# Performance work log

Measured on AMD Instinct MI355X. Metric: run time of the kernel, lower is better.

The kernel has to match this reference:

```python
import jax, jax.numpy as jnp
import numpy as np

N = 8192        # num nodes (bs in the original docstring)
D_IN = 512      # input feature dim
HEADS = 8
DPH = 512 // HEADS  # size_per_head = hidden_size // num_heads
EDGE_P = 0.01   # adjacency density


def setup_inputs() -> dict:
    key = jax.random.key(0)
    k1, k2, k3 = jax.random.split(key, 3)
    H = jax.random.normal(k1, (N, D_IN), dtype=jnp.float32)
    # dense 0/1 adjacency, as passed to the layer before tf.sparse.from_dense
    adj = (jax.random.uniform(k2, (N, N)) < EDGE_P).astype(jnp.float32)
    # Glorot-uniform per-head projection kernels, stacked: (HEADS, D_IN, DPH)
    limit = float(np.sqrt(6.0 / (D_IN + DPH)))
    W = jax.random.uniform(k3, (HEADS, D_IN, DPH), jnp.float32, -limit, limit)
    b = jnp.zeros((HEADS, DPH), jnp.float32)
    return {"H": H, "adj": adj, "W": W, "b": b}


def reference(H, adj, W, b):
    # Per-head dense projection: H_ = H @ W_h  -> (HEADS, N, DPH)
    H_ = jnp.einsum('nd,hde->hne', H, W)
    # NOTE: the original layer computes a sparse sigmoid/softmax attention
    # (f1 + f2^T over adj) but never uses it: head_output uses raw adj.
    # Aggregation: adj @ H_ per head, plus bias; activation = tf.identity.
    out = jnp.einsum('nm,hme->hne', adj, H_) + b[:, None, :]  # (HEADS, N, DPH)
    # Concat heads along feature axis (head 0 first) -> (N, HEADS*DPH)
    return jnp.transpose(out, (1, 0, 2)).reshape(H.shape[0], HEADS * DPH)
```

## Files before the change

### kernel.cpp

```cpp
#include <hip/hip_runtime.h>
#include <hip/hip_bf16.h>

typedef __attribute__((ext_vector_type(8))) short short8;
typedef __attribute__((ext_vector_type(4))) float floatx4;

#define GN 8192
#define GD 512
#define MAXDEG 256
#define GEMM_BLOCKS 512

static __device__ __forceinline__ ushort bf16bits(float x) {
  __hip_bfloat16 h = __float2bfloat16(x);
  return *(ushort*)&h;
}
static __device__ __forceinline__ float bf16f(uint u16) {
  return __uint_as_float(u16 << 16);
}

__global__ void detect_kernel(const uint* __restrict__ H, const uint* __restrict__ W,
                              const uint* __restrict__ adj, const uint* __restrict__ b,
                              int* __restrict__ flags, float* __restrict__ bias) {
  __shared__ int cH, cW, cA, cB;
  const int t = threadIdx.x;
  if (t == 0) { cH = 0; cW = 0; cA = 0; cB = 0; }
  __syncthreads();
  { const uint e = (H[t] >> 7) & 0xFFu; if (e >= 100u && e <= 140u) atomicAdd(&cH, 1); }
  { const uint e = (W[t] >> 7) & 0xFFu; if (e >= 100u && e <= 140u) atomicAdd(&cW, 1); }
  for (int i = t; i < 4096; i += 256)
    if ((adj[i] & 0xFFFFu) == 0x3F80u) atomicAdd(&cA, 1);
  if (b[t] != 0u) atomicAdd(&cB, 1);
  __syncthreads();
  const int hb = cH > 128, wb = cW > 128, ab = cA > 0;
  if (t == 0) { flags[0] = hb; flags[1] = wb; flags[2] = ab; }
  if (cB == 0) {
    bias[t] = 0.0f; bias[t + 256] = 0.0f;
  } else if (wb) {
    const ushort* bs = (const ushort*)b;
    bias[t] = bf16f(bs[t]); bias[t + 256] = bf16f(bs[t + 256]);
  } else {
    const float* bf = (const float*)b;
    bias[t] = bf[t]; bias[t + 256] = bf[t + 256];
  }
}

#define BM 128
#define BN 64
#define BK 64
#define LDK 72

#define SMEM_BYTES (BM * LDK * 2 + BN * LDK * 2)

__global__ __launch_bounds__(256) void fused_kernel(
    const void* __restrict__ Hv, const void* __restrict__ Wv,
    const void* __restrict__ adjv, ushort* __restrict__ HP,
    int* __restrict__ rowcnt, uint2* __restrict__ edges,
    const int* __restrict__ flags) {
  __shared__ __align__(16) unsigned char smem[SMEM_BYTES];

  const int tid = threadIdx.x;

  if (blockIdx.x < GEMM_BLOCKS) {
    ushort* sA = (ushort*)smem;
    ushort* sB = (ushort*)(smem + BM * LDK * 2);
    const int hb = flags[0];
    const int wb = flags[1];
    const int bn = blockIdx.x & 7;
    const int bm = blockIdx.x >> 3;
    const int m0 = bm * BM;
    const int lane = tid & 63;
    const int w = tid >> 6;
    const int wr = w >> 1, wc = w & 1;
    const int l15 = lane & 15, q = lane >> 4;

    floatx4 acc[4][2];
#pragma unroll
    for (int i = 0; i < 4; i++)
#pragma unroll
      for (int j = 0; j < 2; j++) acc[i][j] = (floatx4)0.0f;

    for (int k0 = 0; k0 < GD; k0 += BK) {
      __syncthreads();
      if (hb) {
        const ushort* H16 = (const ushort*)Hv;
        const int r = tid >> 3;
        const int kc = (tid & 7) * 8;
#pragma unroll
        for (int p = 0; p < 4; p++) {
          const int row = r + p * 32;
          const uint4 v = *(const uint4*)(H16 + (size_t)(m0 + row) * GD + k0 + kc);
          *(uint4*)(sA + row * LDK + kc) = v;
        }
      } else {
        const float* H32 = (const float*)Hv;
        const int r0 = tid >> 4;
        const int kc = (tid & 15) * 4;
#pragma unroll
        for (int p = 0; p < 8; p++) {
          const int row = r0 + p * 16;
          const float4 v = *(const float4*)(H32 + (size_t)(m0 + row) * GD + k0 + kc);
          ushort4 o;
          o.x = bf16bits(v.x); o.y = bf16bits(v.y);
          o.z = bf16bits(v.z); o.w = bf16bits(v.w);
          *(ushort4*)(sA + row * LDK + kc) = o;
        }
      }
      if (wb) {
        const ushort* Wh = (const ushort*)Wv + (size_t)bn * (512 * 64);
        const int kk = tid >> 3;
        const int e0 = (tid & 7) * 8;
#pragma unroll
        for (int p = 0; p < 2; p++) {
          const int k = kk + p * 32;
          const uint4 v = *(const uint4*)(Wh + (size_t)(k0 + k) * 64 + e0);
          const ushort* pv = (const ushort*)&v;
#pragma unroll
          for (int j = 0; j < 8; j++) sB[(e0 + j) * LDK + k] = pv[j];
        }
      } else {
        const float* Wh = (const float*)Wv + (size_t)bn * (512 * 64);
        const int kk = tid >> 4;
        const int e0 = (tid & 15) * 4;
#pragma unroll
        for (int p = 0; p < 4; p++) {
          const int k = kk + p * 16;
          const float4 v = *(const float4*)(Wh + (size_t)(k0 + k) * 64 + e0);
          sB[(e0 + 0) * LDK + k] = bf16bits(v.x);
          sB[(e0 + 1) * LDK + k] = bf16bits(v.y);
          sB[(e0 + 2) * LDK + k] = bf16bits(v.z);
          sB[(e0 + 3) * LDK + k] = bf16bits(v.w);
        }
      }
      __syncthreads();
#pragma unroll
      for (int kq = 0; kq < 2; kq++) {
        short8 af[4], bfv[2];
#pragma unroll
        for (int mt = 0; mt < 4; mt++)
          af[mt] = *(const short8*)(sA + (wr * 64 + mt * 16 + l15) * LDK + kq * 32 + q * 8);
#pragma unroll
        for (int ct = 0; ct < 2; ct++)
          bfv[ct] = *(const short8*)(sB + (wc * 32 + ct * 16 + l15) * LDK + kq * 32 + q * 8);
#pragma unroll
        for (int mt = 0; mt < 4; mt++)
#pragma unroll
          for (int ct = 0; ct < 2; ct++)
            acc[mt][ct] = __builtin_amdgcn_mfma_f32_16x16x32_bf16(
                af[mt], bfv[ct], acc[mt][ct], 0, 0, 0);
      }
    }
#pragma unroll
    for (int mt = 0; mt < 4; mt++)
#pragma unroll
      for (int ct = 0; ct < 2; ct++)
#pragma unroll
        for (int r = 0; r < 4; r++) {
          const int row = m0 + wr * 64 + mt * 16 + q * 4 + r;
          const int col = bn * 64 + wc * 32 + ct * 16 + l15;
          HP[(size_t)row * GD + col] = bf16bits(acc[mt][ct][r]);
        }
  } else {
    int* s_idx = (int*)smem;
    float* s_val = (float*)(smem + 1024);
    int* s_cnt = (int*)(smem + 2048);
    const int ab = flags[2];
    const int n = blockIdx.x - GEMM_BLOCKS;
    const int t = tid;
    if (t == 0) *s_cnt = 0;
    __syncthreads();
    if (ab) {
      const ushort* arow = (const ushort*)adjv + (size_t)n * GN;
#pragma unroll
      for (int c = 0; c < 8; c++) {
        const int c0 = c * 1024;
        const uint2 v = *(const uint2*)(arow + c0 + t * 4);
        const uint e[4] = {v.x & 0xFFFFu, v.x >> 16, v.y & 0xFFFFu, v.y >> 16};
#pragma unroll
        for (int j = 0; j < 4; j++)
          if (e[j] != 0u) {
            const int pos = atomicAdd(s_cnt, 1);
            if (pos < MAXDEG) { s_idx[pos] = c0 + t * 4 + j; s_val[pos] = bf16f(e[j]); }
          }
      }
    } else {
      const float* arow = (const float*)adjv + (size_t)n * GN;
#pragma unroll
      for (int c = 0; c < 8; c++) {
        const int c0 = c * 1024;
        const float4 v = *(const float4*)(arow + c0 + t * 4);
        const float pv[4] = {v.x, v.y, v.z, v.w};
#pragma unroll
        for (int j = 0; j < 4; j++)
          if (pv[j] != 0.0f) {
            const int pos = atomicAdd(s_cnt, 1);
            if (pos < MAXDEG) { s_idx[pos] = c0 + t * 4 + j; s_val[pos] = pv[j]; }
          }
      }
    }
    __syncthreads();
    const int cnt = min(*s_cnt, MAXDEG);
    if (t == 0) rowcnt[n] = cnt;
    if (t < cnt) {
      uint2 e; e.x = (uint)s_idx[t]; e.y = __float_as_uint(s_val[t]);
      edges[(size_t)n * MAXDEG + t] = e;
    }
  }
}

__global__ __launch_bounds__(128) void gather_kernel(
    const ushort* __restrict__ HP, const int* __restrict__ rowcnt,
    const uint2* __restrict__ edges, const float* __restrict__ bias,
    float* __restrict__ out) {
  __shared__ int s_idx[MAXDEG];
  __shared__ float s_val[MAXDEG];

  const int b = blockIdx.x;
  const int half = b & 1;
  const int n = b >> 1;
  const int t = threadIdx.x;
  const int cnt = rowcnt[n];

  for (int i = t; i < cnt; i += 128) {
    const uint2 e = edges[(size_t)n * MAXDEG + i];
    s_idx[i] = (int)e.x;
    s_val[i] = __uint_as_float(e.y);
  }
  __syncthreads();

  const uint* HPu = (const uint*)HP;
  const int co = (half << 7) + t;
  float acc0 = 0.0f, acc1 = 0.0f;
  int i = 0;
  for (; i + 4 <= cnt; i += 4) {
    const int m0_ = s_idx[i + 0], m1_ = s_idx[i + 1];
    const int m2_ = s_idx[i + 2], m3_ = s_idx[i + 3];
    const float v0 = s_val[i + 0], v1 = s_val[i + 1];
    const float v2 = s_val[i + 2], v3 = s_val[i + 3];
    const uint u0 = HPu[(size_t)m0_ * 256 + co];
    const uint u1 = HPu[(size_t)m1_ * 256 + co];
    const uint u2 = HPu[(size_t)m2_ * 256 + co];
    const uint u3 = HPu[(size_t)m3_ * 256 + co];
    acc0 += v0 * bf16f(u0 & 0xFFFFu) + v1 * bf16f(u1 & 0xFFFFu);
    acc0 += v2 * bf16f(u2 & 0xFFFFu) + v3 * bf16f(u3 & 0xFFFFu);
    acc1 += v0 * __uint_as_float(u0 & 0xFFFF0000u) + v1 * __uint_as_float(u1 & 0xFFFF0000u);
    acc1 += v2 * __uint_as_float(u2 & 0xFFFF0000u) + v3 * __uint_as_float(u3 & 0xFFFF0000u);
  }
  for (; i < cnt; i++) {
    const int m_ = s_idx[i];
    const float vv = s_val[i];
    const uint u = HPu[(size_t)m_ * 256 + co];
    acc0 += vv * bf16f(u & 0xFFFFu);
    acc1 += vv * __uint_as_float(u & 0xFFFF0000u);
  }

  const float2 bb = ((const float2*)bias)[co];
  float2 o;
  o.x = acc0 + bb.x;
  o.y = acc1 + bb.y;
  ((float2*)out)[(size_t)n * 256 + co] = o;
}

extern "C" void kernel_launch(void* const* d_in, const int* in_sizes, int n_in,
                              void* d_out, int out_size, void* d_ws, size_t ws_size,
                              hipStream_t stream) {
  const void *H = d_in[0], *adj = d_in[1], *W = d_in[2], *b = d_in[3];
  for (int i = 0; i < n_in; i++) {
    const int s = in_sizes[i];
    if (s == GN * GN) adj = d_in[i];
    else if (s == GN * GD) H = d_in[i];
    else if (s == 8 * 512 * 64) W = d_in[i];
    else if (s == 512) b = d_in[i];
  }
  float* out = (float*)d_out;

  char* ws = (char*)d_ws;
  ushort* HP   = (ushort*)ws;
  float*  bias = (float*)(ws + (size_t)GN * GD * 2);
  int*    flags= (int*)(ws + (size_t)GN * GD * 2 + 2048);
  int*  rowcnt = (int*)(ws + (size_t)GN * GD * 2 + 4096);
  uint2* edges = (uint2*)(ws + (size_t)GN * GD * 2 + 4096 + GN * 4);

  detect_kernel<<<1, 256, 0, stream>>>((const uint*)H, (const uint*)W,
                                       (const uint*)adj, (const uint*)b,
                                       flags, bias);
  fused_kernel<<<GEMM_BLOCKS + GN, 256, 0, stream>>>(H, W, adj, HP,
                                                     rowcnt, edges, flags);
  gather_kernel<<<GN * 2, 128, 0, stream>>>(HP, rowcnt, edges, bias, out);
}
```

Before: 432.1 us.

## Split projected features into half-width planes and gather one row per wavefront

The GEMM now writes the bf16 projection into two separate half-width arrays (columns 0-255 and 256-511), so each half-row is a contiguous 512-byte segment. The gather kernel is restructured so that each 64-lane wavefront handles one node's half-row. Each lane loads a uint2 (4 bf16 values) per neighbour and stores a float4, and edges are staged in a per-wave shared buffer with no block barrier. This aims to cut the gather's block count and barrier overhead and to widen memory transactions per neighbour row. The trade-off is fewer in-flight loads per output element and slightly higher register pressure.

```diff
diff --git a/kernel.cpp b/kernel.cpp
--- a/kernel.cpp
+++ b/kernel.cpp
@@ -52,9 +52,9 @@
 
 __global__ __launch_bounds__(256) void fused_kernel(
     const void* __restrict__ Hv, const void* __restrict__ Wv,
-    const void* __restrict__ adjv, ushort* __restrict__ HP,
-    int* __restrict__ rowcnt, uint2* __restrict__ edges,
-    const int* __restrict__ flags) {
+    const void* __restrict__ adjv, ushort* __restrict__ HPlo,
+    ushort* __restrict__ HPhi, int* __restrict__ rowcnt,
+    uint2* __restrict__ edges, const int* __restrict__ flags) {
   __shared__ __align__(16) unsigned char smem[SMEM_BYTES];
 
   const int tid = threadIdx.x;
@@ -148,6 +148,8 @@
                 af[mt], bfv[ct], acc[mt][ct], 0, 0, 0);
       }
     }
+    ushort* HPdst = (bn < 4) ? HPlo : HPhi;
+    const int cbase = (bn & 3) * 64;
 #pragma unroll
     for (int mt = 0; mt < 4; mt++)
 #pragma unroll
@@ -155,8 +157,8 @@
 #pragma unroll
         for (int r = 0; r < 4; r++) {
           const int row = m0 + wr * 64 + mt * 16 + q * 4 + r;
-          const int col = bn * 64 + wc * 32 + ct * 16 + l15;
-          HP[(size_t)row * GD + col] = bf16bits(acc[mt][ct][r]);
+          const int col = cbase + wc * 32 + ct * 16 + l15;
+          HPdst[(size_t)row * 256 + col] = bf16bits(acc[mt][ct][r]);
         }
   } else {
     int* s_idx = (int*)smem;
@@ -206,57 +208,58 @@
   }
 }
 
-__global__ __launch_bounds__(128) void gather_kernel(
-    const ushort* __restrict__ HP, const int* __restrict__ rowcnt,
-    const uint2* __restrict__ edges, const float* __restrict__ bias,
-    float* __restrict__ out) {
-  __shared__ int s_idx[MAXDEG];
-  __shared__ float s_val[MAXDEG];
+__global__ __launch_bounds__(256) void gather_kernel(
+    const ushort* __restrict__ HPlo, const ushort* __restrict__ HPhi,
+    const int* __restrict__ rowcnt, const uint2* __restrict__ edges,
+    const float* __restrict__ bias, float* __restrict__ out) {
+  __shared__ uint2 s_e[4][MAXDEG];
 
   const int b = blockIdx.x;
   const int half = b & 1;
-  const int n = b >> 1;
-  const int t = threadIdx.x;
+  const int w = threadIdx.x >> 6;
+  const int lane = threadIdx.x & 63;
+  const int n = (b >> 1) * 4 + w;
+
   const int cnt = rowcnt[n];
-
-  for (int i = t; i < cnt; i += 128) {
-    const uint2 e = edges[(size_t)n * MAXDEG + i];
-    s_idx[i] = (int)e.x;
-    s_val[i] = __uint_as_float(e.y);
-  }
-  __syncthreads();
-
-  const uint* HPu = (const uint*)HP;
-  const int co = (half << 7) + t;
-  float acc0 = 0.0f, acc1 = 0.0f;
+  for (int i = lane; i < cnt; i += 64)
+    s_e[w][i] = edges[(size_t)n * MAXDEG + i];
+
+  const uint2* HPsrc = (const uint2*)(half ? HPhi : HPlo);
+  float a0 = 0.f, a1 = 0.f, a2 = 0.f, a3 = 0.f;
+
   int i = 0;
   for (; i + 4 <= cnt; i += 4) {
-    const int m0_ = s_idx[i + 0], m1_ = s_idx[i + 1];
-    const int m2_ = s_idx[i + 2], m3_ = s_idx[i + 3];
-    const float v0 = s_val[i + 0], v1 = s_val[i + 1];
-    const float v2 = s_val[i + 2], v3 = s_val[i + 3];
-    const uint u0 = HPu[(size_t)m0_ * 256 + co];
-    const uint u1 = HPu[(size_t)m1_ * 256 + co];
-    const uint u2 = HPu[(size_t)m2_ * 256 + co];
-    const uint u3 = HPu[(size_t)m3_ * 256 + co];
-    acc0 += v0 * bf16f(u0 & 0xFFFFu) + v1 * bf16f(u1 & 0xFFFFu);
-    acc0 += v2 * bf16f(u2 & 0xFFFFu) + v3 * bf16f(u3 & 0xFFFFu);
-    acc1 += v0 * __uint_as_float(u0 & 0xFFFF0000u) + v1 * __uint_as_float(u1 & 0xFFFF0000u);
-    acc1 += v2 * __uint_as_float(u2 & 0xFFFF0000u) + v3 * __uint_as_float(u3 & 0xFFFF0000u);
+    const uint2 e0 = s_e[w][i + 0], e1 = s_e[w][i + 1];
+    const uint2 e2 = s_e[w][i + 2], e3 = s_e[w][i + 3];
+    const uint2 u0 = HPsrc[(size_t)e0.x * 64 + lane];
+    const uint2 u1 = HPsrc[(size_t)e1.x * 64 + lane];
+    const uint2 u2 = HPsrc[(size_t)e2.x * 64 + lane];
+    const uint2 u3 = HPsrc[(size_t)e3.x * 64 + lane];
+    const float v0 = __uint_as_float(e0.y), v1 = __uint_as_float(e1.y);
+    const float v2 = __uint_as_float(e2.y), v3 = __uint_as_float(e3.y);
+    a0 += v0 * bf16f(u0.x & 0xFFFFu) + v1 * bf16f(u1.x & 0xFFFFu)
+        + v2 * bf16f(u2.x & 0xFFFFu) + v3 * bf16f(u3.x & 0xFFFFu);
+    a1 += v0 * __uint_as_float(u0.x & 0xFFFF0000u) + v1 * __uint_as_float(u1.x & 0xFFFF0000u)
+        + v2 * __uint_as_float(u2.x & 0xFFFF0000u) + v3 * __uint_as_float(u3.x & 0xFFFF0000u);
+    a2 += v0 * bf16f(u0.y & 0xFFFFu) + v1 * bf16f(u1.y & 0xFFFFu)
+        + v2 * bf16f(u2.y & 0xFFFFu) + v3 * bf16f(u3.y & 0xFFFFu);
+    a3 += v0 * __uint_as_float(u0.y & 0xFFFF0000u) + v1 * __uint_as_float(u1.y & 0xFFFF0000u)
+        + v2 * __uint_as_float(u2.y & 0xFFFF0000u) + v3 * __uint_as_float(u3.y & 0xFFFF0000u);
   }
   for (; i < cnt; i++) {
-    const int m_ = s_idx[i];
-    const float vv = s_val[i];
-    const uint u = HPu[(size_t)m_ * 256 + co];
-    acc0 += vv * bf16f(u & 0xFFFFu);
-    acc1 += vv * __uint_as_float(u & 0xFFFF0000u);
-  }
-
-  const float2 bb = ((const float2*)bias)[co];
-  float2 o;
-  o.x = acc0 + bb.x;
-  o.y = acc1 + bb.y;
-  ((float2*)out)[(size_t)n * 256 + co] = o;
+    const uint2 e = s_e[w][i];
+    const float v = __uint_as_float(e.y);
+    const uint2 u = HPsrc[(size_t)e.x * 64 + lane];
+    a0 += v * bf16f(u.x & 0xFFFFu);
+    a1 += v * __uint_as_float(u.x & 0xFFFF0000u);
+    a2 += v * bf16f(u.y & 0xFFFFu);
+    a3 += v * __uint_as_float(u.y & 0xFFFF0000u);
+  }
+
+  const float4 bb = ((const float4*)bias)[half * 64 + lane];
+  float4 o;
+  o.x = a0 + bb.x; o.y = a1 + bb.y; o.z = a2 + bb.z; o.w = a3 + bb.w;
+  ((float4*)out)[(size_t)n * 128 + half * 64 + lane] = o;
 }
 
 extern "C" void kernel_launch(void* const* d_in, const int* in_sizes, int n_in,
@@ -273,7 +276,8 @@
   float* out = (float*)d_out;
 
   char* ws = (char*)d_ws;
-  ushort* HP   = (ushort*)ws;
+  ushort* HPlo = (ushort*)ws;
+  ushort* HPhi = (ushort*)(ws + (size_t)GN * 256 * 2);
   float*  bias = (float*)(ws + (size_t)GN * GD * 2);
   int*    flags= (int*)(ws + (size_t)GN * GD * 2 + 2048);
   int*  rowcnt = (int*)(ws + (size_t)GN * GD * 2 + 4096);
@@ -282,7 +286,7 @@
   detect_kernel<<<1, 256, 0, stream>>>((const uint*)H, (const uint*)W,
                                        (const uint*)adj, (const uint*)b,
                                        flags, bias);
-  fused_kernel<<<GEMM_BLOCKS + GN, 256, 0, stream>>>(H, W, adj, HP,
+  fused_kernel<<<GEMM_BLOCKS + GN, 256, 0, stream>>>(H, W, adj, HPlo, HPhi,
                                                      rowcnt, edges, flags);
-  gather_kernel<<<GN * 2, 128, 0, stream>>>(HP, rowcnt, edges, bias, out);
-}
+  gather_kernel<<<GN / 2, 256, 0, stream>>>(HPlo, HPhi, rowcnt, edges, bias, out);
+}
```

Measured after the change: 439.0 us. No clear change (+1.6%).
